# Performance work log

Measured on AMD Instinct MI355X. Metric: run time of the kernel, lower is better.

The kernel has to match this reference:

```python
import jax, jax.numpy as jnp
import numpy as np

NEG = -1e30  # finite stand-in for -inf (keeps grads NaN-free)

def _rnnt_costs(log_probs, labels, lengths, label_lengths):
    """RNN-T negative log-likelihood per example.
    log_probs: (N, T, U, V) log-probabilities; labels: (N, U-1) int32;
    lengths, label_lengths: (N,) int32. blank = V-1 (module default).
    alpha recurrence: alpha[t,u] = LSE(alpha[t-1,u]+blank[t-1,u], alpha[t,u-1]+emit[t,u-1]).
    Each row-in-u linear log-recurrence is solved in parallel with cumlogsumexp:
    alpha[t,u] = c[u] + LSE_{k<=u}(A[k] - c[k]),  c = exclusive cumsum of emit[t], A = alpha[t-1]+blank[t-1].
    """
    N, T, U, V = log_probs.shape
    blank = V - 1
    blank_lp = log_probs[..., blank]  # (N, T, U)
    lbl = jnp.broadcast_to(labels[:, None, :, None], (N, T, U - 1, 1))
    emit = jnp.take_along_axis(log_probs[:, :, : U - 1, :], lbl, axis=3)[..., 0]  # (N, T, U-1)

    def row(A, emit_row):
        # A: (N, U) = alpha[t-1] + blank[t-1]; emit_row: (N, U-1) = emit[t]
        c = jnp.concatenate([jnp.zeros((N, 1), log_probs.dtype),
                             jnp.cumsum(emit_row, axis=1)], axis=1)  # (N, U)
        return c + jax.lax.cumlogsumexp(A - c, axis=1)

    A0 = jnp.full((N, U), NEG, log_probs.dtype).at[:, 0].set(0.0)
    alpha0 = row(A0, emit[:, 0, :])  # row t = 0

    def step(alpha_prev, xs):
        blank_prev, emit_row = xs  # (N, U), (N, U-1)
        alpha = row(alpha_prev + blank_prev, emit_row)
        return alpha, alpha

    xs = (jnp.swapaxes(blank_lp[:, :-1, :], 0, 1),  # (T-1, N, U)
          jnp.swapaxes(emit[:, 1:, :], 0, 1))       # (T-1, N, U-1)
    _, alphas = jax.lax.scan(step, alpha0, xs)
    alphas = jnp.concatenate([alpha0[None], alphas], axis=0)  # (T, N, U)

    n = jnp.arange(N)
    t_idx = lengths.astype(jnp.int32) - 1
    u_idx = label_lengths.astype(jnp.int32)
    loglik = alphas[t_idx, n, u_idx] + blank_lp[n, t_idx, u_idx]
    return -loglik  # (N,)


def setup_inputs() -> dict:
    key = jax.random.key(0)
    k1, k2, k3, k4 = jax.random.split(key, 4)
    N, T, U, V = 16, 256, 128, 256
    logits = jax.random.normal(k1, (N, T, U, V), dtype=jnp.float32)
    log_probs = jax.nn.log_softmax(logits, axis=-1)
    labels = jax.random.randint(k2, (N, U - 1), 0, V - 1, dtype=jnp.int32)  # never blank
    lengths = jax.random.randint(k3, (N,), T // 2, T + 1, dtype=jnp.int32).at[0].set(T)
    label_lengths = jax.random.randint(k4, (N,), (U - 1) // 2, U, dtype=jnp.int32).at[0].set(U - 1)
    return {"log_probs": log_probs, "labels": labels,
            "lengths": lengths, "label_lengths": label_lengths}


def reference(log_probs, labels, lengths, label_lengths):
    costs = _rnnt_costs(log_probs, labels, lengths, label_lengths)
    return jnp.mean(costs)  # reduction='mean'
```

## Files before the change

kernel.cpp:

```cpp
#include <hip/hip_runtime.h>


#define T_DIM 256
#define U_DIM 128
#define V_DIM 256
#define UV (U_DIM * V_DIM)
#define NEGF (-1e30f)

__device__ __forceinline__ float lse2(float x, float y) {
    float m = fmaxf(x, y);
    float mn = fminf(x, y);
    return m + __logf(1.0f + __expf(mn - m));
}

__global__ __launch_bounds__(64, 1) void rnnt_alpha_kernel(
        const float* __restrict__ lp, const int* __restrict__ labels,
        const int* __restrict__ lengths, const int* __restrict__ lab_lens,
        float* __restrict__ out, float inv_n) {
    const int n    = blockIdx.x;
    const int lane = threadIdx.x;
    const int u0   = lane * 2;
    const int u1   = u0 + 1;
    const float* lpn = lp + (size_t)n * (size_t)(T_DIM * UV);

    const int lbl0 = (u0 >= 1) ? labels[n * (U_DIM - 1) + (u0 - 1)] : 0;
    const int lbl1 = labels[n * (U_DIM - 1) + u0];

    const int t_len = lengths[n];
    const int u_len = lab_lens[n];
    const int dstar = (t_len - 1) + u_len;

    const int cb0 = u0 * V_DIM + (V_DIM - 1);
    const int cb1 = u1 * V_DIM + (V_DIM - 1);
    const int ce0 = (u0 - 1) * V_DIM + lbl0;
    const int ce1 = u0 * V_DIM + lbl1;

    float a0 = (lane == 0) ? 0.0f : NEGF;
    float a1 = NEGF;
    float res = NEGF;
    if (dstar == 0 && lane == 0) res = a0;

    float nb = __shfl_up(a1, 1, 64);

    constexpr int PF = 8;
    float bufB0[PF], bufB1[PF], bufE0[PF], bufE1[PF];

    auto issue = [&](int d, int slot) {
        int tb0 = d - 1 - u0;
        int tb1 = d - 1 - u1;
        int te0 = d - u0;
        int te1 = d - u1;
        int c;
        c = min(max(tb0, 0), T_DIM - 1); bufB0[slot] = lpn[c * UV + cb0];
        c = min(max(tb1, 0), T_DIM - 1); bufB1[slot] = lpn[c * UV + cb1];
        c = min(max(te0, 0), T_DIM - 1); bufE0[slot] = lpn[c * UV + ce0];
        c = min(max(te1, 0), T_DIM - 1); bufE1[slot] = lpn[c * UV + ce1];
    };

#pragma unroll
    for (int j = 0; j < PF; ++j) issue(1 + j, j);

    for (int dd = 1; dd < 385; dd += PF) {
#pragma unroll
        for (int j = 0; j < PF; ++j) {
            const int d = dd + j;
            const int t0 = d - u0;
            const int t1 = d - u1;
            const bool vb0 = (unsigned)(t0 - 1) < (unsigned)(T_DIM - 1);
            const bool vb1 = (unsigned)(t1 - 1) < (unsigned)(T_DIM - 1);
            const bool ve0 = (u0 >= 1) && ((unsigned)t0 < (unsigned)T_DIM);
            const bool ve1 = ((unsigned)t1 < (unsigned)T_DIM);

            const float pa0 = vb0 ? (a0 + bufB0[j]) : NEGF;
            const float pb0 = ve0 ? (nb + bufE0[j]) : NEGF;
            const float na0 = lse2(pa0, pb0);

            const float pa1 = vb1 ? (a1 + bufB1[j]) : NEGF;
            const float pb1 = ve1 ? (a0 + bufE1[j]) : NEGF;
            const float na1 = lse2(pa1, pb1);

            a0 = na0;
            a1 = na1;
            nb = __shfl_up(a1, 1, 64);

            issue(d + PF, j);

            if (d == dstar) {
                if (u_len == u0)      res = na0;
                else if (u_len == u1) res = na1;
            }
        }
    }

    if (lane == (u_len >> 1)) {
        const float bl = lpn[(t_len - 1) * UV + u_len * V_DIM + (V_DIM - 1)];
        atomicAdd(out, -(res + bl) * inv_n);
    }
}

extern "C" void kernel_launch(void* const* d_in, const int* in_sizes, int n_in,
                              void* d_out, int out_size, void* d_ws, size_t ws_size,
                              hipStream_t stream) {
    const float* lp      = (const float*)d_in[0];
    const int*   labels  = (const int*)d_in[1];
    const int*   lengths = (const int*)d_in[2];
    const int*   lablens = (const int*)d_in[3];
    float* out = (float*)d_out;
    const int N = in_sizes[2];

    hipMemsetAsync(d_out, 0, sizeof(float), stream);
    rnnt_alpha_kernel<<<dim3(N), dim3(64), 0, stream>>>(
        lp, labels, lengths, lablens, out, 1.0f / (float)N);
}
```

Before: 773.1 us.

## Pre-gather blank/emit log-probs into diagonal-major workspace before the alpha sweep

```diff
diff --git a/kernel.cpp b/kernel.cpp
--- a/kernel.cpp
+++ b/kernel.cpp
@@ -5,6 +5,7 @@
 #define U_DIM 128
 #define V_DIM 256
 #define UV (U_DIM * V_DIM)
+#define E_ROWS 384
 #define NEGF (-1e30f)
 
 __device__ __forceinline__ float lse2(float x, float y) {
@@ -13,27 +14,40 @@
     return m + __logf(1.0f + __expf(mn - m));
 }
 
-__global__ __launch_bounds__(64, 1) void rnnt_alpha_kernel(
+__global__ __launch_bounds__(128) void rnnt_gather_kernel(
         const float* __restrict__ lp, const int* __restrict__ labels,
+        float* __restrict__ Bd, float* __restrict__ Ed) {
+    const int e = blockIdx.x;
+    const int n = blockIdx.y;
+    const int u = threadIdx.x;
+    const int t = e - u;
+    if ((unsigned)t >= (unsigned)T_DIM) return;
+    const float* cell = lp + ((size_t)n * T_DIM + t) * (size_t)UV + u * V_DIM;
+    float* brow = Bd + ((size_t)n * E_ROWS + e) * U_DIM;
+    brow[u] = cell[V_DIM - 1];
+    if (u < U_DIM - 1) {
+        const int lbl = labels[n * (U_DIM - 1) + u];
+        float* erow = Ed + ((size_t)n * E_ROWS + e) * U_DIM;
+        erow[u + 1] = cell[lbl];
+    }
+}
+
+__global__ __launch_bounds__(64, 1) void rnnt_diag_kernel(
+        const float* __restrict__ lp,
+        const float* __restrict__ Bd, const float* __restrict__ Ed,
         const int* __restrict__ lengths, const int* __restrict__ lab_lens,
         float* __restrict__ out, float inv_n) {
     const int n    = blockIdx.x;
     const int lane = threadIdx.x;
     const int u0   = lane * 2;
     const int u1   = u0 + 1;
-    const float* lpn = lp + (size_t)n * (size_t)(T_DIM * UV);
 
-    const int lbl0 = (u0 >= 1) ? labels[n * (U_DIM - 1) + (u0 - 1)] : 0;
-    const int lbl1 = labels[n * (U_DIM - 1) + u0];
+    const float* Bdn = Bd + (size_t)n * E_ROWS * U_DIM;
+    const float* Edn = Ed + (size_t)n * E_ROWS * U_DIM;
 
     const int t_len = lengths[n];
     const int u_len = lab_lens[n];
     const int dstar = (t_len - 1) + u_len;
-
-    const int cb0 = u0 * V_DIM + (V_DIM - 1);
-    const int cb1 = u1 * V_DIM + (V_DIM - 1);
-    const int ce0 = (u0 - 1) * V_DIM + lbl0;
-    const int ce1 = u0 * V_DIM + lbl1;
 
     float a0 = (lane == 0) ? 0.0f : NEGF;
     float a1 = NEGF;
@@ -43,18 +57,14 @@
     float nb = __shfl_up(a1, 1, 64);
 
     constexpr int PF = 8;
-    float bufB0[PF], bufB1[PF], bufE0[PF], bufE1[PF];
+    float2 bufB[PF], bufE[PF];
 
     auto issue = [&](int d, int slot) {
-        int tb0 = d - 1 - u0;
-        int tb1 = d - 1 - u1;
-        int te0 = d - u0;
-        int te1 = d - u1;
-        int c;
-        c = min(max(tb0, 0), T_DIM - 1); bufB0[slot] = lpn[c * UV + cb0];
-        c = min(max(tb1, 0), T_DIM - 1); bufB1[slot] = lpn[c * UV + cb1];
-        c = min(max(te0, 0), T_DIM - 1); bufE0[slot] = lpn[c * UV + ce0];
-        c = min(max(te1, 0), T_DIM - 1); bufE1[slot] = lpn[c * UV + ce1];
+        const int e = min(d - 1, E_ROWS - 1);
+        const float2* br = (const float2*)(Bdn + (size_t)e * U_DIM);
+        const float2* er = (const float2*)(Edn + (size_t)e * U_DIM);
+        bufB[slot] = br[lane];
+        bufE[slot] = er[lane];
     };
 
 #pragma unroll
@@ -71,12 +81,12 @@
             const bool ve0 = (u0 >= 1) && ((unsigned)t0 < (unsigned)T_DIM);
             const bool ve1 = ((unsigned)t1 < (unsigned)T_DIM);
 
-            const float pa0 = vb0 ? (a0 + bufB0[j]) : NEGF;
-            const float pb0 = ve0 ? (nb + bufE0[j]) : NEGF;
+            const float pa0 = vb0 ? (a0 + bufB[j].x) : NEGF;
+            const float pb0 = ve0 ? (nb + bufE[j].x) : NEGF;
             const float na0 = lse2(pa0, pb0);
 
-            const float pa1 = vb1 ? (a1 + bufB1[j]) : NEGF;
-            const float pb1 = ve1 ? (a0 + bufE1[j]) : NEGF;
+            const float pa1 = vb1 ? (a1 + bufB[j].y) : NEGF;
+            const float pb1 = ve1 ? (a0 + bufE[j].y) : NEGF;
             const float na1 = lse2(pa1, pb1);
 
             a0 = na0;
@@ -93,7 +103,8 @@
     }
 
     if (lane == (u_len >> 1)) {
-        const float bl = lpn[(t_len - 1) * UV + u_len * V_DIM + (V_DIM - 1)];
+        const float bl = lp[(size_t)n * T_DIM * UV + (size_t)(t_len - 1) * UV
+                            + u_len * V_DIM + (V_DIM - 1)];
         atomicAdd(out, -(res + bl) * inv_n);
     }
 }
@@ -108,7 +119,12 @@
     float* out = (float*)d_out;
     const int N = in_sizes[2];
 
+    float* Bd = (float*)d_ws;
+    float* Ed = Bd + (size_t)N * E_ROWS * U_DIM;
+
     hipMemsetAsync(d_out, 0, sizeof(float), stream);
-    rnnt_alpha_kernel<<<dim3(N), dim3(64), 0, stream>>>(
-        lp, labels, lengths, lablens, out, 1.0f / (float)N);
+    rnnt_gather_kernel<<<dim3(E_ROWS - 1, N), dim3(128), 0, stream>>>(
+        lp, labels, Bd, Ed);
+    rnnt_diag_kernel<<<dim3(N), dim3(64), 0, stream>>>(
+        lp, Bd, Ed, lengths, lablens, out, 1.0f / (float)N);
 }
```

Result: faster. 671.2 us (-13.2%).
